# Optimization experiments

Hardware: AMD Instinct MI355X
Metric: run time of the kernel (lower is better)

Reference implementation:

```python
import jax, jax.numpy as jnp
import numpy as np

B, N, DIM = 4, 8192, 1024
H, DH, W = 16, 64, 128
INNER = H * DH


def setup_inputs() -> dict:
    key = jax.random.key(0)
    k0, k1, k2, k3 = jax.random.split(key, 4)
    s = 0.02
    return {
        "x": jax.random.normal(k0, (B, N, DIM), jnp.float32),
        "wq": jax.random.normal(k1, (DIM, INNER), jnp.float32) * s,
        "wkv": jax.random.normal(k2, (DIM, 2 * INNER), jnp.float32) * s,
        "wo": jax.random.normal(k3, (INNER, DIM), jnp.float32) * s,
        "bo": jnp.zeros((DIM,), jnp.float32),
    }


def reference(x, wq, wkv, wo, bo):
    b, n, _ = x.shape
    h, dh, w = H, DH, W
    scale = dh ** -0.5
    # projections (n is a multiple of w, so no padding path)
    q = x @ wq
    k, v = jnp.split(x @ wkv, 2, axis=-1)

    def to_windows(t):
        # b n (h d) -> (b h) n d -> (b h) n/w w d
        t = t.reshape(b, n, h, dh).transpose(0, 2, 1, 3)
        return t.reshape(b * h, n // w, w, dh)

    qw, kw, vw = map(to_windows, (q, k, v))

    def add_prev_window(t):
        # prepend a zero window, then each window sees [prev, current] -> j = 2w
        tp = jnp.pad(t, ((0, 0), (1, 0), (0, 0), (0, 0)))
        return jnp.concatenate([tp[:, :-1], tp[:, 1:]], axis=2)

    kw, vw = add_prev_window(kw), add_prev_window(vw)

    sim = jnp.einsum('bwid,bwjd->bwij', qw, kw) * scale  # (bh, n/w, w, 2w)
    i, j = w, 2 * w
    causal = jnp.triu(jnp.ones((i, j), bool), j - i + 1)  # masks j > i + w
    neg = -jnp.finfo(sim.dtype).max
    sim = jnp.where(causal, neg, sim)
    attn = jax.nn.softmax(sim, axis=-1)
    out = jnp.einsum('bwij,bwjd->bwid', attn, vw)  # (bh, n/w, w, dh)
    out = out.reshape(b, h, n, dh).transpose(0, 2, 1, 3).reshape(b, n, h * dh)
    return out @ wo + bo
```

## Files before the change

### kernel.cpp

```cpp
#include <hip/hip_runtime.h>
#include <stdint.h>

typedef unsigned short u16;
typedef __bf16 bf16x8 __attribute__((ext_vector_type(8)));
typedef float f32x4 __attribute__((ext_vector_type(4)));
typedef unsigned short u16x8 __attribute__((ext_vector_type(8)));

#define MFMA16(a, b, c) __builtin_amdgcn_mfma_f32_16x16x32_bf16((a), (b), (c), 0, 0, 0)

#define SEQ_N 8192
#define NWIN 64

#define BAR() __builtin_amdgcn_s_barrier()
#define PRIO1() __builtin_amdgcn_s_setprio(1)
#define PRIO0() __builtin_amdgcn_s_setprio(0)
#define VM8() asm volatile("s_waitcnt vmcnt(8)" ::: "memory")
#define VM0() asm volatile("s_waitcnt vmcnt(0)" ::: "memory")
#define LGKM0() asm volatile("s_waitcnt lgkmcnt(0)" ::: "memory")

__device__ __forceinline__ u16 f2bf(float f) {
  union { float f; uint32_t u; } v; v.f = f;
  return (u16)((v.u + 0x7fffu + ((v.u >> 16) & 1u)) >> 16);
}

__device__ __forceinline__ void load_lds16(const void* g, void* l) {
  __builtin_amdgcn_global_load_lds((const __attribute__((address_space(1))) void*)g,
                                   (__attribute__((address_space(3))) void*)l, 16, 0, 0);
}

__global__ __launch_bounds__(256) void cast_bf16_kernel(const float* __restrict__ src,
                                                        u16* __restrict__ dst, int n8) {
  int i = blockIdx.x * 256 + threadIdx.x;
  if (i >= n8) return;
  const float4* s = (const float4*)src + (size_t)i * 2;
  float4 a = s[0], b = s[1];
  u16x8 o;
  o[0] = f2bf(a.x); o[1] = f2bf(a.y); o[2] = f2bf(a.z); o[3] = f2bf(a.w);
  o[4] = f2bf(b.x); o[5] = f2bf(b.y); o[6] = f2bf(b.z); o[7] = f2bf(b.w);
  *((u16x8*)dst + i) = o;
}

__global__ __launch_bounds__(256) void transpose_cast_kernel(u16* __restrict__ dst,
                                                             const float* __restrict__ srcA,
                                                             const float* __restrict__ srcB,
                                                             int bcols) {
  __shared__ float tile[32][33];
  const int tx = threadIdx.x & 31, ty = threadIdx.x >> 5;
  const int n0 = blockIdx.x * 32, k0 = blockIdx.y * 32;
#pragma unroll
  for (int i = 0; i < 4; ++i) {
    int k = k0 + ty + i * 8;
    int n = n0 + tx;
    float v = (n < 1024) ? srcA[(size_t)k * 1024 + n]
                         : srcB[(size_t)k * bcols + (n - 1024)];
    tile[ty + i * 8][tx] = v;
  }
  __syncthreads();
#pragma unroll
  for (int i = 0; i < 4; ++i) {
    int n = n0 + ty + i * 8;
    int k = k0 + tx;
    dst[(size_t)n * 1024 + k] = f2bf(tile[tx][ty + i * 8]);
  }
}

#define READ_A(MH)                                                                 \
  _Pragma("unroll") for (int kk = 0; kk < 2; ++kk)                                 \
  _Pragma("unroll") for (int m = 0; m < 4; ++m)                                    \
    af[m][kk] = *(const bf16x8*)(Ard + bo + (((MH) * 64 + m * 16) << 7) + ax[kk]);

#define READ_B(NH)                                                                 \
  _Pragma("unroll") for (int kk = 0; kk < 2; ++kk)                                 \
  _Pragma("unroll") for (int n = 0; n < 2; ++n)                                    \
    bfr[n][kk] = *(const bf16x8*)(Brd + bo + (((NH) * 32 + n * 16) << 7) + ax[kk]);

#define MFMA_QUAD(MH, NH)                                                          \
  _Pragma("unroll") for (int kk = 0; kk < 2; ++kk)                                 \
  _Pragma("unroll") for (int m = 0; m < 4; ++m)                                    \
  _Pragma("unroll") for (int n = 0; n < 2; ++n)                                    \
    acc[(MH) * 4 + m][(NH) * 2 + n] =                                              \
        MFMA16(af[m][kk], bfr[n][kk], acc[(MH) * 4 + m][(NH) * 2 + n]);

template <int NBN, int MODE>
__global__ __launch_bounds__(512, 2) void gemm8_kernel(
    const u16* __restrict__ A, const u16* __restrict__ Bt,
    u16* __restrict__ qo, u16* __restrict__ ko, u16* __restrict__ vo,
    float* __restrict__ out, const float* __restrict__ bias) {
  extern __shared__ char smem[];
  constexpr int K = 1024;
  constexpr int NT = K / 64;
  const int tid = threadIdx.x;
  const int wave = tid >> 6, lane = tid & 63;
  const int quad = lane >> 4, l15 = lane & 15;
  const int wm = wave >> 2, wn = wave & 3;

  const int idx0 = blockIdx.x;
  const int local = idx0 >> 3;
  const int bn = local >> 4;
  const int bm = ((idx0 & 7) << 4) + (local & 15);

  char* const Ab = smem;
  char* const Bb = smem + 65536;

  const int sr = lane >> 3;
  const int sg = ((lane & 7) ^ sr) * 8;
  const u16* const gA = A + (size_t)(bm * 256 + wave * 32 + sr) * K + sg;
  const u16* const gB = Bt + (size_t)(bn * 256 + wave * 32 + sr) * K + sg;
  char* const lA = Ab + wave * 32 * 128;
  char* const lB = Bb + wave * 32 * 128;

  auto stage = [&](int buf, int kt) {
#pragma unroll
    for (int i = 0; i < 4; ++i)
      load_lds16(gA + (size_t)kt * 64 + i * 8 * K, lA + buf * 32768 + i * 1024);
#pragma unroll
    for (int i = 0; i < 4; ++i)
      load_lds16(gB + (size_t)kt * 64 + i * 8 * K, lB + buf * 32768 + i * 1024);
  };

  const int ax[2] = { (quad ^ (l15 & 7)) << 4, ((quad ^ (l15 & 7)) << 4) ^ 64 };
  const char* const Ard = Ab + ((wm * 128 + l15) << 7);
  const char* const Brd = Bb + ((wn * 64 + l15) << 7);

  f32x4 acc[8][4] = {};
  bf16x8 af[4][2], bfr[2][2];

  stage(0, 0);
  stage(1, 1);
  VM8();
  BAR();

  for (int kt = 0; kt < NT; ++kt) {
    const int buf = kt & 1;
    const int bo = buf * 32768;
    READ_A(0)
    READ_B(0)
    BAR(); LGKM0();
    PRIO1(); MFMA_QUAD(0, 0) PRIO0();
    BAR();
    READ_B(1)
    BAR(); LGKM0();
    PRIO1(); MFMA_QUAD(0, 1) PRIO0();
    BAR();
    READ_A(1)
    BAR(); LGKM0();
    PRIO1(); MFMA_QUAD(1, 1) PRIO0();
    BAR();
    READ_B(0)
    LGKM0();
    BAR();
    if (kt + 2 < NT) stage(buf, kt + 2);
    PRIO1(); MFMA_QUAD(1, 0) PRIO0();
    if (kt < NT - 1) {
      if (kt + 2 < NT) { VM8(); } else { VM0(); }
      BAR();
    }
  }

  const int row0 = bm * 256 + wm * 128;
#pragma unroll
  for (int mt = 0; mt < 8; ++mt) {
#pragma unroll
    for (int nt = 0; nt < 4; ++nt) {
      if (MODE == 0) {
        u16* dst = (bn < 4) ? qo : ((bn < 8) ? ko : vo);
        const int cc = ((bn & 3) << 8) + wn * 64 + nt * 16 + l15;
#pragma unroll
        for (int r = 0; r < 4; ++r) {
          const int row = row0 + mt * 16 + quad * 4 + r;
          dst[(size_t)row * 1024 + cc] = f2bf(acc[mt][nt][r]);
        }
      } else {
        const int col = bn * 256 + wn * 64 + nt * 16 + l15;
        const float bv = bias[col];
#pragma unroll
        for (int r = 0; r < 4; ++r) {
          const int row = row0 + mt * 16 + quad * 4 + r;
          out[(size_t)row * 1024 + col] = acc[mt][nt][r] + bv;
        }
      }
    }
  }
}

__global__ __launch_bounds__(256, 2) void attn_kernel(const u16* __restrict__ qb,
                                                      const u16* __restrict__ kb,
                                                      const u16* __restrict__ vb,
                                                      u16* __restrict__ ob) {
  __shared__ u16 Vt[64][264];
  __shared__ u16 Ps[4 * 2048];
  const int tid = threadIdx.x;
  const int wave = tid >> 6, lane = tid & 63;
  const int quad = lane >> 4, l15 = lane & 15;
  const int blk = blockIdx.x;
  const int wi = blk & (NWIN - 1);
  const int bh = blk >> 6;
  const long tok0 = (long)(bh >> 4) * SEQ_N + (long)wi * 128;
  const int hoff = (bh & 15) * 64;
  const long qbase = tok0 * 1024 + hoff;
  const long kbase = (tok0 - 128) * 1024 + hoff;

  {
    const int t = tid;
    const bool pad = (wi == 0) && (t < 128);
#pragma unroll
    for (int d0 = 0; d0 < 64; d0 += 8) {
      u16x8 v8;
      if (pad) {
        v8 = (u16x8)0;
      } else {
        v8 = *(const u16x8*)(vb + (kbase + (long)t * 1024 + d0));
      }
#pragma unroll
      for (int j = 0; j < 8; ++j) Vt[d0 + j][t] = v8[j];
    }
  }

  bf16x8 qf[2][2];
#pragma unroll
  for (int mt = 0; mt < 2; ++mt)
#pragma unroll
    for (int kk = 0; kk < 2; ++kk)
      qf[mt][kk] = *(const bf16x8*)(qb + (qbase + (long)(wave * 32 + mt * 16 + l15) * 1024 +
                                          kk * 32 + quad * 8));

  f32x4 s[2][16] = {};
#pragma unroll
  for (int nt = 0; nt < 16; ++nt) {
    if (!((wi == 0) && (nt < 8))) {
      const long kt = kbase + (long)(nt * 16 + l15) * 1024;
      bf16x8 kf0 = *(const bf16x8*)(kb + (kt + quad * 8));
      bf16x8 kf1 = *(const bf16x8*)(kb + (kt + 32 + quad * 8));
#pragma unroll
      for (int mt = 0; mt < 2; ++mt) {
        s[mt][nt] = MFMA16(qf[mt][0], kf0, s[mt][nt]);
        s[mt][nt] = MFMA16(qf[mt][1], kf1, s[mt][nt]);
      }
    }
  }

#pragma unroll
  for (int mt = 0; mt < 2; ++mt) {
#pragma unroll
    for (int r = 0; r < 4; ++r) {
      const int row = wave * 32 + mt * 16 + quad * 4 + r;
      float m = -3.0e38f;
#pragma unroll
      for (int nt = 0; nt < 16; ++nt) {
        const int col = nt * 16 + l15;
        float x = s[mt][nt][r] * 0.125f;
        if (col > row + 128) x = -3.0e38f;
        s[mt][nt][r] = x;
        m = fmaxf(m, x);
      }
      m = fmaxf(m, __shfl_xor(m, 1));
      m = fmaxf(m, __shfl_xor(m, 2));
      m = fmaxf(m, __shfl_xor(m, 4));
      m = fmaxf(m, __shfl_xor(m, 8));
      float sum = 0.f;
#pragma unroll
      for (int nt = 0; nt < 16; ++nt) {
        float e = __expf(s[mt][nt][r] - m);
        s[mt][nt][r] = e;
        sum += e;
      }
      sum += __shfl_xor(sum, 1);
      sum += __shfl_xor(sum, 2);
      sum += __shfl_xor(sum, 4);
      sum += __shfl_xor(sum, 8);
      const float inv = 1.0f / sum;
#pragma unroll
      for (int nt = 0; nt < 16; ++nt) s[mt][nt][r] *= inv;
    }
  }

  __syncthreads();

  f32x4 o[2][4] = {};
#pragma unroll
  for (int ks = 0; ks < 8; ++ks) {
    u16* myP = &Ps[wave * 2048 + (ks & 1) * 1024];
#pragma unroll
    for (int mt = 0; mt < 2; ++mt)
#pragma unroll
      for (int half = 0; half < 2; ++half) {
        const int nt = ks * 2 + half;
#pragma unroll
        for (int r = 0; r < 4; ++r)
          myP[(mt * 16 + quad * 4 + r) * 32 + half * 16 + l15] = f2bf(s[mt][nt][r]);
      }
    bf16x8 pf[2];
    pf[0] = *(const bf16x8*)&myP[l15 * 32 + quad * 8];
    pf[1] = *(const bf16x8*)&myP[(16 + l15) * 32 + quad * 8];
#pragma unroll
    for (int ont = 0; ont < 4; ++ont) {
      bf16x8 vf = *(const bf16x8*)&Vt[ont * 16 + l15][ks * 32 + quad * 8];
      o[0][ont] = MFMA16(pf[0], vf, o[0][ont]);
      o[1][ont] = MFMA16(pf[1], vf, o[1][ont]);
    }
  }

#pragma unroll
  for (int mt = 0; mt < 2; ++mt)
#pragma unroll
    for (int ont = 0; ont < 4; ++ont)
#pragma unroll
      for (int r = 0; r < 4; ++r) {
        const int row = wave * 32 + mt * 16 + quad * 4 + r;
        const int col = ont * 16 + l15;
        ob[qbase + (long)row * 1024 + col] = f2bf(o[mt][ont][r]);
      }
}

extern "C" void kernel_launch(void* const* d_in, const int* in_sizes, int n_in,
                              void* d_out, int out_size, void* d_ws, size_t ws_size,
                              hipStream_t stream) {
  const float* x   = (const float*)d_in[0];
  const float* wq  = (const float*)d_in[1];
  const float* wkv = (const float*)d_in[2];
  const float* wo  = (const float*)d_in[3];
  const float* bo  = (const float*)d_in[4];
  float* out = (float*)d_out;

  const size_t XE = (size_t)4 * SEQ_N * 1024;
  u16* ws = (u16*)d_ws;
  u16* xb    = ws;
  u16* qbuf  = ws + XE;
  u16* kbuf  = ws + 2 * XE;
  u16* vbuf  = ws + 3 * XE;
  u16* wqkvT = ws + 4 * XE;
  u16* woT   = wqkvT + 3072 * 1024;
  u16* obuf  = xb;

  hipFuncSetAttribute(reinterpret_cast<const void*>(gemm8_kernel<12, 0>),
                      hipFuncAttributeMaxDynamicSharedMemorySize, 131072);
  hipFuncSetAttribute(reinterpret_cast<const void*>(gemm8_kernel<4, 1>),
                      hipFuncAttributeMaxDynamicSharedMemorySize, 131072);

  cast_bf16_kernel<<<16384, 256, 0, stream>>>(x, xb, (int)(XE / 8));
  transpose_cast_kernel<<<dim3(96, 32), 256, 0, stream>>>(wqkvT, wq, wkv, 2048);
  transpose_cast_kernel<<<dim3(32, 32), 256, 0, stream>>>(woT, wo, wo, 1024);
  gemm8_kernel<12, 0><<<1536, 512, 131072, stream>>>(xb, wqkvT, qbuf, kbuf, vbuf,
                                                     nullptr, nullptr);
  attn_kernel<<<4096, 256, 0, stream>>>(qbuf, kbuf, vbuf, obuf);
  gemm8_kernel<4, 1><<<512, 512, 131072, stream>>>(obuf, woT, nullptr, nullptr, nullptr,
                                                   out, bo);
}
```

Baseline: 660.9 us.

## Double-register LDS fragments in GEMM main loop and remap attention block order

Restructures the GEMM k-loop to load both B halves and the second A half into separate register fragments, so each LDS read phase overlaps the preceding MFMA group and several barriers and lgkmcnt waits go away. Sched barriers pin the instruction order. Separately, the attention kernel's block index is permuted so that consecutive dispatched blocks spread across XCDs, which is meant to improve cache locality. The extra fragment registers raise VGPR pressure and could hurt occupancy at launch bounds 512,2.

```diff
diff --git a/kernel.cpp b/kernel.cpp
--- a/kernel.cpp
+++ b/kernel.cpp
@@ -14,6 +14,7 @@
 #define BAR() __builtin_amdgcn_s_barrier()
 #define PRIO1() __builtin_amdgcn_s_setprio(1)
 #define PRIO0() __builtin_amdgcn_s_setprio(0)
+#define SB0() __builtin_amdgcn_sched_barrier(0)
 #define VM8() asm volatile("s_waitcnt vmcnt(8)" ::: "memory")
 #define VM0() asm volatile("s_waitcnt vmcnt(0)" ::: "memory")
 #define LGKM0() asm volatile("s_waitcnt lgkmcnt(0)" ::: "memory")
@@ -64,22 +65,22 @@
   }
 }
 
-#define READ_A(MH)                                                                 \
+#define READ_A_TO(dst, MH)                                                         \
   _Pragma("unroll") for (int kk = 0; kk < 2; ++kk)                                 \
   _Pragma("unroll") for (int m = 0; m < 4; ++m)                                    \
-    af[m][kk] = *(const bf16x8*)(Ard + bo + (((MH) * 64 + m * 16) << 7) + ax[kk]);
-
-#define READ_B(NH)                                                                 \
+    dst[m][kk] = *(const bf16x8*)(Ard + bo + (((MH) * 64 + m * 16) << 7) + ax[kk]);
+
+#define READ_B_TO(dst, NH)                                                         \
   _Pragma("unroll") for (int kk = 0; kk < 2; ++kk)                                 \
   _Pragma("unroll") for (int n = 0; n < 2; ++n)                                    \
-    bfr[n][kk] = *(const bf16x8*)(Brd + bo + (((NH) * 32 + n * 16) << 7) + ax[kk]);
-
-#define MFMA_QUAD(MH, NH)                                                          \
+    dst[n][kk] = *(const bf16x8*)(Brd + bo + (((NH) * 32 + n * 16) << 7) + ax[kk]);
+
+#define MFMAQ(fa, fb, MH, NH)                                                      \
   _Pragma("unroll") for (int kk = 0; kk < 2; ++kk)                                 \
   _Pragma("unroll") for (int m = 0; m < 4; ++m)                                    \
   _Pragma("unroll") for (int n = 0; n < 2; ++n)                                    \
     acc[(MH) * 4 + m][(NH) * 2 + n] =                                              \
-        MFMA16(af[m][kk], bfr[n][kk], acc[(MH) * 4 + m][(NH) * 2 + n]);
+        MFMA16(fa[m][kk], fb[n][kk], acc[(MH) * 4 + m][(NH) * 2 + n]);
 
 template <int NBN, int MODE>
 __global__ __launch_bounds__(512, 2) void gemm8_kernel(
@@ -123,7 +124,7 @@
   const char* const Brd = Bb + ((wn * 64 + l15) << 7);
 
   f32x4 acc[8][4] = {};
-  bf16x8 af[4][2], bfr[2][2];
+  bf16x8 afA[4][2], afB[4][2], bf0[2][2], bf1[2][2];
 
   stage(0, 0);
   stage(1, 1);
@@ -131,26 +132,22 @@
   BAR();
 
   for (int kt = 0; kt < NT; ++kt) {
-    const int buf = kt & 1;
-    const int bo = buf * 32768;
-    READ_A(0)
-    READ_B(0)
-    BAR(); LGKM0();
-    PRIO1(); MFMA_QUAD(0, 0) PRIO0();
+    const int bo = (kt & 1) * 32768;
+    READ_A_TO(afA, 0)
+    READ_B_TO(bf0, 0)
+    READ_B_TO(bf1, 1)
+    SB0();
+    PRIO1(); MFMAQ(afA, bf0, 0, 0) PRIO0();
     BAR();
-    READ_B(1)
-    BAR(); LGKM0();
-    PRIO1(); MFMA_QUAD(0, 1) PRIO0();
+    READ_A_TO(afB, 1)
+    SB0();
+    PRIO1(); MFMAQ(afA, bf1, 0, 1) PRIO0();
     BAR();
-    READ_A(1)
-    BAR(); LGKM0();
-    PRIO1(); MFMA_QUAD(1, 1) PRIO0();
-    BAR();
-    READ_B(0)
+    PRIO1(); MFMAQ(afB, bf1, 1, 1) PRIO0();
     LGKM0();
     BAR();
-    if (kt + 2 < NT) stage(buf, kt + 2);
-    PRIO1(); MFMA_QUAD(1, 0) PRIO0();
+    if (kt + 2 < NT) stage(kt & 1, kt + 2);
+    PRIO1(); MFMAQ(afB, bf0, 1, 0) PRIO0();
     if (kt < NT - 1) {
       if (kt + 2 < NT) { VM8(); } else { VM0(); }
       BAR();
@@ -192,7 +189,8 @@
   const int tid = threadIdx.x;
   const int wave = tid >> 6, lane = tid & 63;
   const int quad = lane >> 4, l15 = lane & 15;
-  const int blk = blockIdx.x;
+  const int raw = blockIdx.x;
+  const int blk = ((raw & 7) << 9) | (raw >> 3);
   const int wi = blk & (NWIN - 1);
   const int bh = blk >> 6;
   const long tok0 = (long)(bh >> 4) * SEQ_N + (long)wi * 128;
```

Measured after the change: 644.9 us. 1.02x faster.
